# Performance work log

Hardware: AMD Instinct MI355X
Metric: run time of the kernel (lower is better)

Reference implementation:

```python
import jax, jax.numpy as jnp
import numpy as np

N = 100_000      # nodes
E = 1_600_000    # edges (avg degree 16)
D = 64           # num_features == dim == edge_dim
L = 3            # num_layers
G = 512          # graphs in batch
BN_EPS = 1e-5


def setup_inputs() -> dict:
    key = jax.random.key(0)
    ks = jax.random.split(key, 12)
    s = 0.1  # weight init scale
    x = jax.random.normal(ks[0], (N, D), jnp.float32)
    edge_attr = jax.random.normal(ks[1], (E, D), jnp.float32)
    edge_index = jax.random.randint(ks[2], (2, E), 0, N)
    batch = jnp.sort(jax.random.randint(ks[3], (N,), 0, G))
    # stacked per-layer params (all layers same shape since num_features == dim)
    We = jax.random.normal(ks[4], (L, D, D), jnp.float32) * s   # GINEConv edge Linear
    be = jax.random.normal(ks[5], (L, D), jnp.float32) * s
    W1 = jax.random.normal(ks[6], (L, D, D), jnp.float32) * s   # mlp Linear 1
    b1 = jax.random.normal(ks[7], (L, D), jnp.float32) * s
    W2 = jax.random.normal(ks[8], (L, D, D), jnp.float32) * s   # mlp Linear 2
    b2 = jax.random.normal(ks[9], (L, D), jnp.float32) * s
    gamma = jnp.ones((L, D), jnp.float32)                       # BatchNorm affine
    beta = jnp.zeros((L, D), jnp.float32)
    return dict(x=x, edge_attr=edge_attr, We=We, be=be, W1=W1, b1=b1,
                W2=W2, b2=b2, gamma=gamma, beta=beta,
                edge_index=edge_index, batch=batch)


def reference(x, edge_attr, We, be, W1, b1, W2, b2, gamma, beta, edge_index, batch):
    src, dst = edge_index[0], edge_index[1]
    pooled = []
    h = x
    for l in range(L):
        # GINEConv: message = ReLU(x_src + edge_lin(edge_attr)), sum-aggregate at dst
        e = edge_attr @ We[l] + be[l]                      # [E, D]
        m = jax.nn.relu(h[src] + e)                        # [E, D] gather + add + relu
        agg = jax.ops.segment_sum(m, dst, num_segments=N)  # [N, D] scatter-sum
        z = h + agg                                        # (1+eps)*x with eps=0
        # GINE mlp: Linear -> ReLU -> Linear
        z = jax.nn.relu(z @ W1[l] + b1[l]) @ W2[l] + b2[l]
        # block: ReLU then BatchNorm1d (training mode: batch stats, biased var)
        z = jax.nn.relu(z)
        mu = z.mean(axis=0)
        var = jnp.mean((z - mu) ** 2, axis=0)
        h = gamma[l] * (z - mu) * jax.lax.rsqrt(var + BN_EPS) + beta[l]
        # global_add_pool over graphs
        pooled.append(jax.ops.segment_sum(h, batch, num_segments=G))
    return jnp.concatenate(pooled, axis=1), h
```

## Files before the change

kernel.cpp:

```cpp
#include <hip/hip_runtime.h>
#include <hip/hip_bf16.h>

#define NN 100000
#define NE 1600000
#define DD 64
#define NG 512
#define POOLED_F (NG * 3 * DD)
#define STATS_F  (3 * 128)
#define SCAN_NB 196

typedef unsigned short u16;
typedef __attribute__((ext_vector_type(8))) short bf16x8;
typedef __attribute__((ext_vector_type(4))) float f32x4;

__device__ __forceinline__ float bf2f(u16 u) {
    return __uint_as_float(((unsigned)u) << 16);
}
__device__ __forceinline__ u16 f2bf(float f) {
    unsigned b = __float_as_uint(f);
    return (u16)((b + 0x7FFFu + ((b >> 16) & 1u)) >> 16);
}

__global__ __launch_bounds__(256) void k_zero(float* __restrict__ p, int n) {
    int i = blockIdx.x * 256 + threadIdx.x;
    if (i < n) p[i] = 0.f;
}
__global__ __launch_bounds__(256) void k_zeroi(int* __restrict__ p, int n) {
    int i = blockIdx.x * 256 + threadIdx.x;
    if (i < n) p[i] = 0;
}
__global__ __launch_bounds__(256) void k_sentinel(float* out, float val) {
    if (threadIdx.x == 0 && blockIdx.x == 0) out[0] = val;
}

__global__ __launch_bounds__(256) void k_hist(const int* __restrict__ dst,
                                              int* __restrict__ counts) {
    int e = blockIdx.x * 256 + threadIdx.x;
    if (e < NE) atomicAdd(&counts[dst[e]], 1);
}

__global__ __launch_bounds__(512) void k_scanA(const int* __restrict__ counts,
                                               int* __restrict__ bsum) {
    __shared__ int red[512];
    int tid = threadIdx.x;
    int idx = blockIdx.x * 512 + tid;
    red[tid] = (idx < NN) ? counts[idx] : 0;
    __syncthreads();
    for (int w = 256; w > 0; w >>= 1) {
        if (tid < w) red[tid] += red[tid + w];
        __syncthreads();
    }
    if (tid == 0) bsum[blockIdx.x] = red[0];
}

__global__ __launch_bounds__(256) void k_scanB(const int* __restrict__ bsum,
                                               int* __restrict__ boff,
                                               int* __restrict__ rowptr) {
    __shared__ int sh[256];
    int tid = threadIdx.x;
    int v = (tid < SCAN_NB) ? bsum[tid] : 0;
    sh[tid] = v;
    __syncthreads();
    for (int off = 1; off < 256; off <<= 1) {
        int t = (tid >= off) ? sh[tid - off] : 0;
        __syncthreads();
        sh[tid] += t;
        __syncthreads();
    }
    if (tid < SCAN_NB) boff[tid] = sh[tid] - v;
    if (tid == SCAN_NB - 1) rowptr[NN] = sh[tid];
}

__global__ __launch_bounds__(512) void k_scanC(const int* __restrict__ counts,
                                               const int* __restrict__ boff,
                                               int* __restrict__ rowptr,
                                               int* __restrict__ cursor) {
    __shared__ int sh[512];
    int tid = threadIdx.x;
    int idx = blockIdx.x * 512 + tid;
    int v = (idx < NN) ? counts[idx] : 0;
    sh[tid] = v;
    __syncthreads();
    for (int off = 1; off < 512; off <<= 1) {
        int t = (tid >= off) ? sh[tid - off] : 0;
        __syncthreads();
        sh[tid] += t;
        __syncthreads();
    }
    if (idx < NN) {
        int r = boff[blockIdx.x] + sh[tid] - v;
        rowptr[idx] = r;
        cursor[idx] = r;
    }
}

__global__ __launch_bounds__(256) void k_scatter(const int* __restrict__ src,
                                                 const int* __restrict__ dst,
                                                 int* __restrict__ cursor,
                                                 int* __restrict__ epos,
                                                 int* __restrict__ psrc) {
    int e = blockIdx.x * 256 + threadIdx.x;
    if (e >= NE) return;
    int pos = atomicAdd(&cursor[dst[e]], 1);
    epos[e] = pos;
    psrc[pos] = src[e];
}

__global__ __launch_bounds__(256) void k_fmsg(
    const float* __restrict__ ea, const float* __restrict__ We,
    const float* __restrict__ be, const int* __restrict__ epos,
    u16* __restrict__ msgb)
{
    __shared__ u16 stage[4][16][72];
    int tid = threadIdx.x;
    int wv = tid >> 6, lane = tid & 63;
    int lg = lane >> 4, lr = lane & 15;

    bf16x8 wf[3][4][2];
    float bias[3][4];
#pragma unroll
    for (int l = 0; l < 3; ++l)
#pragma unroll
        for (int cb = 0; cb < 4; ++cb) {
#pragma unroll
            for (int kh = 0; kh < 2; ++kh) {
                bf16x8 f;
#pragma unroll
                for (int j = 0; j < 8; ++j) {
                    int k = kh * 32 + lg * 8 + j;
                    f[j] = (short)f2bf(We[l * 4096 + k * 64 + cb * 16 + lr]);
                }
                wf[l][cb][kh] = f;
            }
            bias[l][cb] = be[l * 64 + cb * 16 + lr];
        }

    const int ngroups = NE / 16;
    for (int g = blockIdx.x * 4 + wv; g < ngroups; g += gridDim.x * 4) {
        int ebase = g * 16;
        bf16x8 af[2];
#pragma unroll
        for (int kh = 0; kh < 2; ++kh) {
            const float4* ap =
                (const float4*)(ea + (size_t)(ebase + lr) * DD + kh * 32 + lg * 8);
            float4 t0 = ap[0], t1 = ap[1];
            bf16x8 f;
            f[0] = (short)f2bf(t0.x); f[1] = (short)f2bf(t0.y);
            f[2] = (short)f2bf(t0.z); f[3] = (short)f2bf(t0.w);
            f[4] = (short)f2bf(t1.x); f[5] = (short)f2bf(t1.y);
            f[6] = (short)f2bf(t1.z); f[7] = (short)f2bf(t1.w);
            af[kh] = f;
        }
#pragma unroll
        for (int l = 0; l < 3; ++l) {
#pragma unroll
            for (int cb = 0; cb < 4; ++cb) {
                f32x4 acc = {0.f, 0.f, 0.f, 0.f};
                acc = __builtin_amdgcn_mfma_f32_16x16x32_bf16(
                          af[0], wf[l][cb][0], acc, 0, 0, 0);
                acc = __builtin_amdgcn_mfma_f32_16x16x32_bf16(
                          af[1], wf[l][cb][1], acc, 0, 0, 0);
#pragma unroll
                for (int i = 0; i < 4; ++i)
                    stage[wv][lg * 4 + i][cb * 16 + lr] =
                        f2bf(acc[i] + bias[l][cb]);
            }
#pragma unroll
            for (int p = 0; p < 2; ++p) {
                int row = p * 8 + (lane >> 3), chunk = lane & 7;
                uint4 v = *(const uint4*)&stage[wv][row][chunk * 8];
                int pos = epos[ebase + row];
                *(uint4*)(msgb + ((size_t)l * NE + pos) * DD + chunk * 8) = v;
            }
        }
    }
}

__global__ __launch_bounds__(256) void k_agg(
    const u16* __restrict__ msgb, const float* __restrict__ h,
    const int* __restrict__ rowptr, const int* __restrict__ psrc,
    float* __restrict__ agg)
{
    int node = (blockIdx.x * 256 + threadIdx.x) >> 6;
    int lane = threadIdx.x & 63;
    if (node >= NN) return;
    int beg = rowptr[node], end = rowptr[node + 1];
    float acc = h[(size_t)node * DD + lane];
    int j = beg;
    for (; j + 3 < end; j += 4) {
        int s0 = psrc[j], s1 = psrc[j + 1], s2 = psrc[j + 2], s3 = psrc[j + 3];
        float m0 = h[(size_t)s0 * DD + lane] + bf2f(msgb[(size_t)j * DD + lane]);
        float m1 = h[(size_t)s1 * DD + lane] + bf2f(msgb[(size_t)(j + 1) * DD + lane]);
        float m2 = h[(size_t)s2 * DD + lane] + bf2f(msgb[(size_t)(j + 2) * DD + lane]);
        float m3 = h[(size_t)s3 * DD + lane] + bf2f(msgb[(size_t)(j + 3) * DD + lane]);
        acc += fmaxf(m0, 0.f) + fmaxf(m1, 0.f) + fmaxf(m2, 0.f) + fmaxf(m3, 0.f);
    }
    for (; j < end; ++j) {
        int s = psrc[j];
        acc += fmaxf(h[(size_t)s * DD + lane] + bf2f(msgb[(size_t)j * DD + lane]), 0.f);
    }
    agg[(size_t)node * DD + lane] = acc;
}

__global__ __launch_bounds__(256) void k_mlp(
    const float* in, const float* __restrict__ W1, const float* __restrict__ b1,
    const float* __restrict__ W2, const float* __restrict__ b2, float* out)
{
    __shared__ __align__(16) float W1l[DD * DD];
    __shared__ __align__(16) float W2l[DD * DD];
    __shared__ __align__(16) float b1l[DD];
    __shared__ __align__(16) float b2l[DD];
    int tid = threadIdx.x;
    for (int i = tid; i < DD * DD / 4; i += 256) {
        ((float4*)W1l)[i] = ((const float4*)W1)[i];
        ((float4*)W2l)[i] = ((const float4*)W2)[i];
    }
    if (tid < DD / 4) {
        ((float4*)b1l)[tid] = ((const float4*)b1)[tid];
        ((float4*)b2l)[tid] = ((const float4*)b2)[tid];
    }
    __syncthreads();

    int n = blockIdx.x * 256 + tid;
    if (n >= NN) return;

    float xr[DD];
    const float4* inrow = (const float4*)(in + (size_t)n * DD);
#pragma unroll
    for (int i = 0; i < DD / 4; ++i) {
        float4 t = inrow[i];
        xr[4*i] = t.x; xr[4*i+1] = t.y; xr[4*i+2] = t.z; xr[4*i+3] = t.w;
    }
    float z1[DD];
    for (int c4 = 0; c4 < DD / 4; ++c4) {
        float4 acc = ((float4*)b1l)[c4];
#pragma unroll
        for (int k = 0; k < DD; ++k) {
            float4 w = ((float4*)W1l)[k * (DD/4) + c4];
            acc.x = fmaf(xr[k], w.x, acc.x);
            acc.y = fmaf(xr[k], w.y, acc.y);
            acc.z = fmaf(xr[k], w.z, acc.z);
            acc.w = fmaf(xr[k], w.w, acc.w);
        }
        z1[c4*4+0] = fmaxf(acc.x, 0.f);
        z1[c4*4+1] = fmaxf(acc.y, 0.f);
        z1[c4*4+2] = fmaxf(acc.z, 0.f);
        z1[c4*4+3] = fmaxf(acc.w, 0.f);
    }
    float4* outrow = (float4*)(out + (size_t)n * DD);
    for (int c4 = 0; c4 < DD / 4; ++c4) {
        float4 acc = ((float4*)b2l)[c4];
#pragma unroll
        for (int k = 0; k < DD; ++k) {
            float4 w = ((float4*)W2l)[k * (DD/4) + c4];
            acc.x = fmaf(z1[k], w.x, acc.x);
            acc.y = fmaf(z1[k], w.y, acc.y);
            acc.z = fmaf(z1[k], w.z, acc.z);
            acc.w = fmaf(z1[k], w.w, acc.w);
        }
        float4 o;
        o.x = fmaxf(acc.x, 0.f); o.y = fmaxf(acc.y, 0.f);
        o.z = fmaxf(acc.z, 0.f); o.w = fmaxf(acc.w, 0.f);
        outrow[c4] = o;
    }
}

__global__ __launch_bounds__(256) void k_stats(const float* __restrict__ z,
                                               float* __restrict__ stats) {
    int tid = threadIdx.x;
    int c = tid & 63;
    float s = 0.f, s2 = 0.f;
    for (int n = blockIdx.x * 4 + (tid >> 6); n < NN; n += 1024) {
        float v = z[(size_t)n * DD + c];
        s += v;
        s2 = fmaf(v, v, s2);
    }
    __shared__ float red[512];
    red[tid] = s; red[256 + tid] = s2;
    __syncthreads();
    if (tid < 64) {
        float a = red[tid] + red[64+tid] + red[128+tid] + red[192+tid];
        float b = red[256+tid] + red[320+tid] + red[384+tid] + red[448+tid];
        atomicAdd(&stats[c], a);
        atomicAdd(&stats[64 + c], b);
    }
}

__global__ void k_bnfinal(float* __restrict__ stats,
                          const float* __restrict__ gamma,
                          const float* __restrict__ beta) {
    int c = threadIdx.x;
    float mu  = stats[c] * (1.0f / NN);
    float var = stats[64 + c] * (1.0f / NN) - mu * mu;
    float rstd = rsqrtf(var + 1e-5f);
    float sc = gamma[c] * rstd;
    stats[c] = sc;
    stats[64 + c] = beta[c] - sc * mu;
}

__global__ __launch_bounds__(256) void k_norm_pool(
    const float* __restrict__ z, const float* __restrict__ stats,
    const int* __restrict__ batch, float* __restrict__ hout,
    float* __restrict__ pooled, int l)
{
    int wave = (blockIdx.x * 256 + threadIdx.x) >> 6;
    int lane = threadIdx.x & 63;
    int n0 = wave * 64;
    if (n0 >= NN) return;
    int n1 = n0 + 64; if (n1 > NN) n1 = NN;
    float sc = stats[lane], sh = stats[64 + lane];
    int gcur = batch[n0];
    float acc = 0.f;
    for (int n = n0; n < n1; ++n) {
        float h = fmaf(z[(size_t)n * DD + lane], sc, sh);
        hout[(size_t)n * DD + lane] = h;
        int g = batch[n];
        if (g != gcur) {
            atomicAdd(&pooled[(size_t)gcur * (3 * DD) + l * DD + lane], acc);
            gcur = g; acc = 0.f;
        }
        acc += h;
    }
    atomicAdd(&pooled[(size_t)gcur * (3 * DD) + l * DD + lane], acc);
}

__global__ __launch_bounds__(256) void k_copy(const float* __restrict__ src,
                                              float* __restrict__ agg) {
    int total = NN * DD / 4;
    for (int i = blockIdx.x * 256 + threadIdx.x; i < total; i += gridDim.x * 256)
        ((float4*)agg)[i] = ((const float4*)src)[i];
}
__global__ __launch_bounds__(256) void k_edge(
    const float* __restrict__ ea, const float* __restrict__ h,
    const float* __restrict__ W, const float* __restrict__ bias,
    const int* __restrict__ src, const int* __restrict__ dst,
    float* __restrict__ agg)
{
    __shared__ __align__(16) float Wl[DD * DD];
    __shared__ __align__(16) float bl[DD];
    int tid = threadIdx.x;
    for (int i = tid; i < DD * DD / 4; i += 256)
        ((float4*)Wl)[i] = ((const float4*)W)[i];
    if (tid < DD / 4) ((float4*)bl)[tid] = ((const float4*)bias)[tid];
    __syncthreads();
    int e = blockIdx.x * 256 + tid;
    int s = src[e], d = dst[e];
    float av[DD];
    const float4* earow = (const float4*)(ea + (size_t)e * DD);
#pragma unroll
    for (int i = 0; i < DD / 4; ++i) {
        float4 t = earow[i];
        av[4*i] = t.x; av[4*i+1] = t.y; av[4*i+2] = t.z; av[4*i+3] = t.w;
    }
    const float4* hrow = (const float4*)(h + (size_t)s * DD);
    float* arow = agg + (size_t)d * DD;
    for (int c4 = 0; c4 < DD / 4; ++c4) {
        float4 acc = ((float4*)bl)[c4];
#pragma unroll
        for (int k = 0; k < DD; ++k) {
            float4 w = ((float4*)Wl)[k * (DD/4) + c4];
            acc.x = fmaf(av[k], w.x, acc.x);
            acc.y = fmaf(av[k], w.y, acc.y);
            acc.z = fmaf(av[k], w.z, acc.z);
            acc.w = fmaf(av[k], w.w, acc.w);
        }
        float4 hv = hrow[c4];
        atomicAdd(arow + c4*4 + 0, fmaxf(hv.x + acc.x, 0.f));
        atomicAdd(arow + c4*4 + 1, fmaxf(hv.y + acc.y, 0.f));
        atomicAdd(arow + c4*4 + 2, fmaxf(hv.z + acc.z, 0.f));
        atomicAdd(arow + c4*4 + 3, fmaxf(hv.w + acc.w, 0.f));
    }
}

extern "C" void kernel_launch(void* const* d_in, const int* in_sizes, int n_in,
                              void* d_out, int out_size, void* d_ws, size_t ws_size,
                              hipStream_t stream) {
    const float* x     = (const float*)d_in[0];
    const float* ea    = (const float*)d_in[1];
    const float* We    = (const float*)d_in[2];
    const float* be    = (const float*)d_in[3];
    const float* W1    = (const float*)d_in[4];
    const float* b1    = (const float*)d_in[5];
    const float* W2    = (const float*)d_in[6];
    const float* b2    = (const float*)d_in[7];
    const float* gamma = (const float*)d_in[8];
    const float* beta  = (const float*)d_in[9];
    const int*   eidx  = (const int*)d_in[10];
    const int*   batch = (const int*)d_in[11];
    const int* src = eidx;
    const int* dst = eidx + NE;

    float* out_pool = (float*)d_out;
    float* out_h    = out_pool + POOLED_F;

    const int exp_sizes[12] = {6400000, 102400000, 12288, 192, 12288, 192,
                               12288, 192, 192, 192, 3200000, 100000};
    bool ok = (n_in == 12);
    for (int i = 0; ok && i < 12; ++i) ok = (in_sizes[i] == exp_sizes[i]);
    if (!ok) {
        k_sentinel<<<1, 64, 0, stream>>>((float*)d_out, 16384.0f);
        return;
    }

    u16*   msgb   = (u16*)d_ws;
    float* agg    = (float*)(msgb + (size_t)3 * NE * DD);
    float* stats  = agg + (size_t)NN * DD;
    int*   rowptr = (int*)(stats + STATS_F);
    int*   cursor = rowptr + (NN + 1);
    int*   counts = cursor + NN;
    int*   epos   = counts + NN;
    int*   psrc   = epos + NE;
    int*   bsum   = psrc + NE;
    int*   boff   = bsum + 256;
    size_t needed_fast = (size_t)3 * NE * DD * 2
                       + ((size_t)NN * DD + STATS_F) * 4
                       + ((size_t)(NN + 1) + NN + NN + NE + NE + 512) * 4;

    k_zero<<<(POOLED_F + 255) / 256, 256, 0, stream>>>(out_pool, POOLED_F);

    if (ws_size >= needed_fast) {
        k_zero<<<(STATS_F + 255) / 256, 256, 0, stream>>>(stats, STATS_F);
        k_zeroi<<<(NN + 255) / 256, 256, 0, stream>>>(counts, NN);
        k_hist<<<NE / 256, 256, 0, stream>>>(dst, counts);
        k_scanA<<<SCAN_NB, 512, 0, stream>>>(counts, bsum);
        k_scanB<<<1, 256, 0, stream>>>(bsum, boff, rowptr);
        k_scanC<<<SCAN_NB, 512, 0, stream>>>(counts, boff, rowptr, cursor);
        k_scatter<<<NE / 256, 256, 0, stream>>>(src, dst, cursor, epos, psrc);

        k_fmsg<<<2048, 256, 0, stream>>>(ea, We, be, epos, msgb);

        for (int l = 0; l < 3; ++l) {
            const float* h = (l == 0) ? x : out_h;
            const u16* msg_l = msgb + (size_t)l * NE * DD;
            k_agg<<<(NN * DD + 255) / 256, 256, 0, stream>>>(msg_l, h, rowptr,
                                                             psrc, agg);
            k_mlp<<<(NN + 255) / 256, 256, 0, stream>>>(agg, W1 + l * DD * DD,
                                                        b1 + l * DD,
                                                        W2 + l * DD * DD,
                                                        b2 + l * DD, agg);
            k_stats<<<256, 256, 0, stream>>>(agg, stats + l * 128);
            k_bnfinal<<<1, 64, 0, stream>>>(stats + l * 128, gamma + l * DD,
                                            beta + l * DD);
            k_norm_pool<<<(NN + 255) / 256, 256, 0, stream>>>(agg, stats + l * 128,
                                                              batch, out_h,
                                                              out_pool, l);
        }
    } else {
        float* agg2   = (float*)d_ws;
        float* stats2 = agg2 + (size_t)NN * DD;
        if (ws_size < ((size_t)NN * DD + STATS_F) * sizeof(float)) {
            k_sentinel<<<1, 64, 0, stream>>>((float*)d_out, 32768.0f);
            return;
        }
        k_zero<<<(STATS_F + 255) / 256, 256, 0, stream>>>(stats2, STATS_F);
        for (int l = 0; l < 3; ++l) {
            const float* h = (l == 0) ? x : out_h;
            k_copy<<<2048, 256, 0, stream>>>(h, agg2);
            k_edge<<<NE / 256, 256, 0, stream>>>(ea, h, We + l * DD * DD,
                                                 be + l * DD, src, dst, agg2);
            k_mlp<<<(NN + 255) / 256, 256, 0, stream>>>(agg2, W1 + l * DD * DD,
                                                        b1 + l * DD,
                                                        W2 + l * DD * DD,
                                                        b2 + l * DD, agg2);
            k_stats<<<256, 256, 0, stream>>>(agg2, stats2 + l * 128);
            k_bnfinal<<<1, 64, 0, stream>>>(stats2 + l * 128, gamma + l * DD,
                                            beta + l * DD);
            k_norm_pool<<<(NN + 255) / 256, 256, 0, stream>>>(agg2, stats2 + l * 128,
                                                              batch, out_h,
                                                              out_pool, l);
        }
    }
}
```

Before: 1.083 ms.

## Fuse aggregation, MLP and BN statistics into one persistent node kernel

```diff
diff --git a/kernel.cpp b/kernel.cpp
--- a/kernel.cpp
+++ b/kernel.cpp
@@ -176,32 +176,162 @@
     }
 }
 
-__global__ __launch_bounds__(256) void k_agg(
+__global__ __launch_bounds__(256) void k_node(
     const u16* __restrict__ msgb, const float* __restrict__ h,
     const int* __restrict__ rowptr, const int* __restrict__ psrc,
+    const float* __restrict__ W1, const float* __restrict__ b1,
+    const float* __restrict__ W2, const float* __restrict__ b2,
+    float* __restrict__ z, float* __restrict__ stats)
+{
+    __shared__ __align__(16) float zin[4][DD];
+    __shared__ float red[512];
+    int tid = threadIdx.x;
+    int wv = tid >> 6, lane = tid & 63;
+
+    float W1r[DD], W2r[DD];
+#pragma unroll
+    for (int k = 0; k < DD; ++k) {
+        W1r[k] = W1[k * DD + lane];
+        W2r[k] = W2[k * DD + lane];
+    }
+    float b1c = b1[lane], b2c = b2[lane];
+
+    int wid = blockIdx.x * 4 + wv;
+    int nw  = gridDim.x * 4;
+    float s = 0.f, s2 = 0.f;
+
+    for (int node = wid; node < NN; node += nw) {
+        int beg = rowptr[node], end = rowptr[node + 1];
+        float acc = h[(size_t)node * DD + lane];
+        int j = beg;
+        for (; j + 3 < end; j += 4) {
+            int s0 = psrc[j], s1 = psrc[j + 1], s2i = psrc[j + 2], s3 = psrc[j + 3];
+            float m0 = h[(size_t)s0 * DD + lane] + bf2f(msgb[(size_t)j * DD + lane]);
+            float m1 = h[(size_t)s1 * DD + lane] + bf2f(msgb[(size_t)(j + 1) * DD + lane]);
+            float m2 = h[(size_t)s2i * DD + lane] + bf2f(msgb[(size_t)(j + 2) * DD + lane]);
+            float m3 = h[(size_t)s3 * DD + lane] + bf2f(msgb[(size_t)(j + 3) * DD + lane]);
+            acc += fmaxf(m0, 0.f) + fmaxf(m1, 0.f) + fmaxf(m2, 0.f) + fmaxf(m3, 0.f);
+        }
+        for (; j < end; ++j) {
+            int sj = psrc[j];
+            acc += fmaxf(h[(size_t)sj * DD + lane] + bf2f(msgb[(size_t)j * DD + lane]), 0.f);
+        }
+        zin[wv][lane] = acc;
+        float z1 = b1c;
+#pragma unroll
+        for (int kq = 0; kq < DD / 4; ++kq) {
+            float4 q = ((const float4*)zin[wv])[kq];
+            z1 = fmaf(q.x, W1r[kq * 4 + 0], z1);
+            z1 = fmaf(q.y, W1r[kq * 4 + 1], z1);
+            z1 = fmaf(q.z, W1r[kq * 4 + 2], z1);
+            z1 = fmaf(q.w, W1r[kq * 4 + 3], z1);
+        }
+        z1 = fmaxf(z1, 0.f);
+        zin[wv][lane] = z1;
+        float z2 = b2c;
+#pragma unroll
+        for (int kq = 0; kq < DD / 4; ++kq) {
+            float4 q = ((const float4*)zin[wv])[kq];
+            z2 = fmaf(q.x, W2r[kq * 4 + 0], z2);
+            z2 = fmaf(q.y, W2r[kq * 4 + 1], z2);
+            z2 = fmaf(q.z, W2r[kq * 4 + 2], z2);
+            z2 = fmaf(q.w, W2r[kq * 4 + 3], z2);
+        }
+        z2 = fmaxf(z2, 0.f);
+        z[(size_t)node * DD + lane] = z2;
+        s += z2;
+        s2 = fmaf(z2, z2, s2);
+    }
+    red[tid] = s; red[256 + tid] = s2;
+    __syncthreads();
+    if (tid < 64) {
+        float a = red[tid] + red[64 + tid] + red[128 + tid] + red[192 + tid];
+        float b = red[256 + tid] + red[320 + tid] + red[384 + tid] + red[448 + tid];
+        atomicAdd(&stats[tid], a);
+        atomicAdd(&stats[64 + tid], b);
+    }
+}
+
+__global__ __launch_bounds__(256) void k_norm_pool(
+    const float* __restrict__ z, const float* __restrict__ stats,
+    const float* __restrict__ gamma, const float* __restrict__ beta,
+    const int* __restrict__ batch, float* __restrict__ hout,
+    float* __restrict__ pooled, int l)
+{
+    int wave = (blockIdx.x * 256 + threadIdx.x) >> 6;
+    int lane = threadIdx.x & 63;
+    int n0 = wave * 64;
+    if (n0 >= NN) return;
+    int n1 = n0 + 64; if (n1 > NN) n1 = NN;
+
+    float mu  = stats[lane] * (1.0f / NN);
+    float var = stats[64 + lane] * (1.0f / NN) - mu * mu;
+    float rstd = rsqrtf(var + 1e-5f);
+    float sc = gamma[l * DD + lane] * rstd;
+    float sh = beta[l * DD + lane] - sc * mu;
+
+    int gcur = batch[n0];
+    float acc = 0.f;
+    for (int n = n0; n < n1; ++n) {
+        float hv = fmaf(z[(size_t)n * DD + lane], sc, sh);
+        hout[(size_t)n * DD + lane] = hv;
+        int g = batch[n];
+        if (g != gcur) {
+            atomicAdd(&pooled[(size_t)gcur * (3 * DD) + l * DD + lane], acc);
+            gcur = g; acc = 0.f;
+        }
+        acc += hv;
+    }
+    atomicAdd(&pooled[(size_t)gcur * (3 * DD) + l * DD + lane], acc);
+}
+
+__global__ __launch_bounds__(256) void k_copy(const float* __restrict__ src,
+                                              float* __restrict__ agg) {
+    int total = NN * DD / 4;
+    for (int i = blockIdx.x * 256 + threadIdx.x; i < total; i += gridDim.x * 256)
+        ((float4*)agg)[i] = ((const float4*)src)[i];
+}
+__global__ __launch_bounds__(256) void k_edge(
+    const float* __restrict__ ea, const float* __restrict__ h,
+    const float* __restrict__ W, const float* __restrict__ bias,
+    const int* __restrict__ src, const int* __restrict__ dst,
     float* __restrict__ agg)
 {
-    int node = (blockIdx.x * 256 + threadIdx.x) >> 6;
-    int lane = threadIdx.x & 63;
-    if (node >= NN) return;
-    int beg = rowptr[node], end = rowptr[node + 1];
-    float acc = h[(size_t)node * DD + lane];
-    int j = beg;
-    for (; j + 3 < end; j += 4) {
-        int s0 = psrc[j], s1 = psrc[j + 1], s2 = psrc[j + 2], s3 = psrc[j + 3];
-        float m0 = h[(size_t)s0 * DD + lane] + bf2f(msgb[(size_t)j * DD + lane]);
-        float m1 = h[(size_t)s1 * DD + lane] + bf2f(msgb[(size_t)(j + 1) * DD + lane]);
-        float m2 = h[(size_t)s2 * DD + lane] + bf2f(msgb[(size_t)(j + 2) * DD + lane]);
-        float m3 = h[(size_t)s3 * DD + lane] + bf2f(msgb[(size_t)(j + 3) * DD + lane]);
-        acc += fmaxf(m0, 0.f) + fmaxf(m1, 0.f) + fmaxf(m2, 0.f) + fmaxf(m3, 0.f);
-    }
-    for (; j < end; ++j) {
-        int s = psrc[j];
-        acc += fmaxf(h[(size_t)s * DD + lane] + bf2f(msgb[(size_t)j * DD + lane]), 0.f);
-    }
-    agg[(size_t)node * DD + lane] = acc;
-}
-
+    __shared__ __align__(16) float Wl[DD * DD];
+    __shared__ __align__(16) float bl[DD];
+    int tid = threadIdx.x;
+    for (int i = tid; i < DD * DD / 4; i += 256)
+        ((float4*)Wl)[i] = ((const float4*)W)[i];
+    if (tid < DD / 4) ((float4*)bl)[tid] = ((const float4*)bias)[tid];
+    __syncthreads();
+    int e = blockIdx.x * 256 + tid;
+    int s = src[e], d = dst[e];
+    float av[DD];
+    const float4* earow = (const float4*)(ea + (size_t)e * DD);
+#pragma unroll
+    for (int i = 0; i < DD / 4; ++i) {
+        float4 t = earow[i];
+        av[4*i] = t.x; av[4*i+1] = t.y; av[4*i+2] = t.z; av[4*i+3] = t.w;
+    }
+    const float4* hrow = (const float4*)(h + (size_t)s * DD);
+    float* arow = agg + (size_t)d * DD;
+    for (int c4 = 0; c4 < DD / 4; ++c4) {
+        float4 acc = ((float4*)bl)[c4];
+#pragma unroll
+        for (int k = 0; k < DD; ++k) {
+            float4 w = ((float4*)Wl)[k * (DD/4) + c4];
+            acc.x = fmaf(av[k], w.x, acc.x);
+            acc.y = fmaf(av[k], w.y, acc.y);
+            acc.z = fmaf(av[k], w.z, acc.z);
+            acc.w = fmaf(av[k], w.w, acc.w);
+        }
+        float4 hv = hrow[c4];
+        atomicAdd(arow + c4*4 + 0, fmaxf(hv.x + acc.x, 0.f));
+        atomicAdd(arow + c4*4 + 1, fmaxf(hv.y + acc.y, 0.f));
+        atomicAdd(arow + c4*4 + 2, fmaxf(hv.z + acc.z, 0.f));
+        atomicAdd(arow + c4*4 + 3, fmaxf(hv.w + acc.w, 0.f));
+    }
+}
 __global__ __launch_bounds__(256) void k_mlp(
     const float* in, const float* __restrict__ W1, const float* __restrict__ b1,
     const float* __restrict__ W2, const float* __restrict__ b2, float* out)
@@ -220,10 +350,8 @@
         ((float4*)b2l)[tid] = ((const float4*)b2)[tid];
     }
     __syncthreads();
-
     int n = blockIdx.x * 256 + tid;
     if (n >= NN) return;
-
     float xr[DD];
     const float4* inrow = (const float4*)(in + (size_t)n * DD);
 #pragma unroll
@@ -264,7 +392,6 @@
         outrow[c4] = o;
     }
 }
-
 __global__ __launch_bounds__(256) void k_stats(const float* __restrict__ z,
                                                float* __restrict__ stats) {
     int tid = threadIdx.x;
@@ -283,92 +410,6 @@
         float b = red[256+tid] + red[320+tid] + red[384+tid] + red[448+tid];
         atomicAdd(&stats[c], a);
         atomicAdd(&stats[64 + c], b);
-    }
-}
-
-__global__ void k_bnfinal(float* __restrict__ stats,
-                          const float* __restrict__ gamma,
-                          const float* __restrict__ beta) {
-    int c = threadIdx.x;
-    float mu  = stats[c] * (1.0f / NN);
-    float var = stats[64 + c] * (1.0f / NN) - mu * mu;
-    float rstd = rsqrtf(var + 1e-5f);
-    float sc = gamma[c] * rstd;
-    stats[c] = sc;
-    stats[64 + c] = beta[c] - sc * mu;
-}
-
-__global__ __launch_bounds__(256) void k_norm_pool(
-    const float* __restrict__ z, const float* __restrict__ stats,
-    const int* __restrict__ batch, float* __restrict__ hout,
-    float* __restrict__ pooled, int l)
-{
-    int wave = (blockIdx.x * 256 + threadIdx.x) >> 6;
-    int lane = threadIdx.x & 63;
-    int n0 = wave * 64;
-    if (n0 >= NN) return;
-    int n1 = n0 + 64; if (n1 > NN) n1 = NN;
-    float sc = stats[lane], sh = stats[64 + lane];
-    int gcur = batch[n0];
-    float acc = 0.f;
-    for (int n = n0; n < n1; ++n) {
-        float h = fmaf(z[(size_t)n * DD + lane], sc, sh);
-        hout[(size_t)n * DD + lane] = h;
-        int g = batch[n];
-        if (g != gcur) {
-            atomicAdd(&pooled[(size_t)gcur * (3 * DD) + l * DD + lane], acc);
-            gcur = g; acc = 0.f;
-        }
-        acc += h;
-    }
-    atomicAdd(&pooled[(size_t)gcur * (3 * DD) + l * DD + lane], acc);
-}
-
-__global__ __launch_bounds__(256) void k_copy(const float* __restrict__ src,
-                                              float* __restrict__ agg) {
-    int total = NN * DD / 4;
-    for (int i = blockIdx.x * 256 + threadIdx.x; i < total; i += gridDim.x * 256)
-        ((float4*)agg)[i] = ((const float4*)src)[i];
-}
-__global__ __launch_bounds__(256) void k_edge(
-    const float* __restrict__ ea, const float* __restrict__ h,
-    const float* __restrict__ W, const float* __restrict__ bias,
-    const int* __restrict__ src, const int* __restrict__ dst,
-    float* __restrict__ agg)
-{
-    __shared__ __align__(16) float Wl[DD * DD];
-    __shared__ __align__(16) float bl[DD];
-    int tid = threadIdx.x;
-    for (int i = tid; i < DD * DD / 4; i += 256)
-        ((float4*)Wl)[i] = ((const float4*)W)[i];
-    if (tid < DD / 4) ((float4*)bl)[tid] = ((const float4*)bias)[tid];
-    __syncthreads();
-    int e = blockIdx.x * 256 + tid;
-    int s = src[e], d = dst[e];
-    float av[DD];
-    const float4* earow = (const float4*)(ea + (size_t)e * DD);
-#pragma unroll
-    for (int i = 0; i < DD / 4; ++i) {
-        float4 t = earow[i];
-        av[4*i] = t.x; av[4*i+1] = t.y; av[4*i+2] = t.z; av[4*i+3] = t.w;
-    }
-    const float4* hrow = (const float4*)(h + (size_t)s * DD);
-    float* arow = agg + (size_t)d * DD;
-    for (int c4 = 0; c4 < DD / 4; ++c4) {
-        float4 acc = ((float4*)bl)[c4];
-#pragma unroll
-        for (int k = 0; k < DD; ++k) {
-            float4 w = ((float4*)Wl)[k * (DD/4) + c4];
-            acc.x = fmaf(av[k], w.x, acc.x);
-            acc.y = fmaf(av[k], w.y, acc.y);
-            acc.z = fmaf(av[k], w.z, acc.z);
-            acc.w = fmaf(av[k], w.w, acc.w);
-        }
-        float4 hv = hrow[c4];
-        atomicAdd(arow + c4*4 + 0, fmaxf(hv.x + acc.x, 0.f));
-        atomicAdd(arow + c4*4 + 1, fmaxf(hv.y + acc.y, 0.f));
-        atomicAdd(arow + c4*4 + 2, fmaxf(hv.z + acc.z, 0.f));
-        atomicAdd(arow + c4*4 + 3, fmaxf(hv.w + acc.w, 0.f));
     }
 }
 
@@ -403,8 +444,8 @@
     }
 
     u16*   msgb   = (u16*)d_ws;
-    float* agg    = (float*)(msgb + (size_t)3 * NE * DD);
-    float* stats  = agg + (size_t)NN * DD;
+    float* zbuf   = (float*)(msgb + (size_t)3 * NE * DD);
+    float* stats  = zbuf + (size_t)NN * DD;
     int*   rowptr = (int*)(stats + STATS_F);
     int*   cursor = rowptr + (NN + 1);
     int*   counts = cursor + NN;
@@ -432,18 +473,12 @@
         for (int l = 0; l < 3; ++l) {
             const float* h = (l == 0) ? x : out_h;
             const u16* msg_l = msgb + (size_t)l * NE * DD;
-            k_agg<<<(NN * DD + 255) / 256, 256, 0, stream>>>(msg_l, h, rowptr,
-                                                             psrc, agg);
-            k_mlp<<<(NN + 255) / 256, 256, 0, stream>>>(agg, W1 + l * DD * DD,
-                                                        b1 + l * DD,
-                                                        W2 + l * DD * DD,
-                                                        b2 + l * DD, agg);
-            k_stats<<<256, 256, 0, stream>>>(agg, stats + l * 128);
-            k_bnfinal<<<1, 64, 0, stream>>>(stats + l * 128, gamma + l * DD,
-                                            beta + l * DD);
-            k_norm_pool<<<(NN + 255) / 256, 256, 0, stream>>>(agg, stats + l * 128,
-                                                              batch, out_h,
-                                                              out_pool, l);
+            k_node<<<2048, 256, 0, stream>>>(msg_l, h, rowptr, psrc,
+                                             W1 + l * DD * DD, b1 + l * DD,
+                                             W2 + l * DD * DD, b2 + l * DD,
+                                             zbuf, stats + l * 128);
+            k_norm_pool<<<(NN + 255) / 256, 256, 0, stream>>>(
+                zbuf, stats + l * 128, gamma, beta, batch, out_h, out_pool, l);
         }
     } else {
         float* agg2   = (float*)d_ws;
@@ -463,11 +498,8 @@
                                                         W2 + l * DD * DD,
                                                         b2 + l * DD, agg2);
             k_stats<<<256, 256, 0, stream>>>(agg2, stats2 + l * 128);
-            k_bnfinal<<<1, 64, 0, stream>>>(stats2 + l * 128, gamma + l * DD,
-                                            beta + l * DD);
-            k_norm_pool<<<(NN + 255) / 256, 256, 0, stream>>>(agg2, stats2 + l * 128,
-                                                              batch, out_h,
-                                                              out_pool, l);
-        }
-    }
-}
+            k_norm_pool<<<(NN + 255) / 256, 256, 0, stream>>>(
+                agg2, stats2 + l * 128, gamma, beta, batch, out_h, out_pool, l);
+        }
+    }
+}
```

Result: slower. 1.242 ms (+14.7%).
